# Performance work log

Hardware: AMD Instinct MI355X
Metric: run time of the kernel (lower is better)

Reference implementation:

```python
import jax, jax.numpy as jnp
import numpy as np

S, B, H, N = 512, 32, 512, 131072  # seq_len, batch, hidden_dim, num candidate spans
MAX_STEP = 20  # max_length


def setup_inputs() -> dict:
    key = jax.random.key(0)
    ks = jax.random.split(key, 8)
    hidden = jax.random.normal(ks[0], (S, B, 2 * H), dtype=jnp.float32)
    span_bids = jax.random.randint(ks[1], (N,), 0, B, dtype=jnp.int32)
    # begin in [1, S-1-MAX_STEP-1] so that begin-1>=0 and end=begin+step <= S-1
    span_begins = jax.random.randint(ks[2], (N,), 1, S - MAX_STEP - 2, dtype=jnp.int32)
    steps = jax.random.randint(ks[3], (N,), 2, MAX_STEP + 1, dtype=jnp.int32)
    span_ends = span_begins + steps
    span_flags = jax.random.randint(ks[4], (N,), 0, 2, dtype=jnp.int32)
    span_weights = jax.random.uniform(ks[5], (N,), dtype=jnp.float32)
    W1 = jax.random.normal(ks[6], (2 * H, H), dtype=jnp.float32) / np.sqrt(2.0 * H)
    b1 = jnp.zeros((H,), dtype=jnp.float32)
    W2 = jax.random.normal(ks[7], (H, 1), dtype=jnp.float32) / np.sqrt(float(H))
    b2 = jnp.zeros((1,), dtype=jnp.float32)
    return {"hidden": hidden, "span_bids": span_bids, "span_begins": span_begins,
            "span_ends": span_ends, "span_flags": span_flags, "span_weights": span_weights,
            "W1": W1, "b1": b1, "W2": W2, "b2": b2}


def reference(hidden, span_bids, span_begins, span_ends, span_flags, span_weights, W1, b1, W2, b2):
    h = W2.shape[0]  # hidden_dim
    # vectorized _span_embed: fwd diff on first half, bwd diff on second half
    fwd = hidden[span_ends - 1, span_bids, :h] - hidden[span_begins - 1, span_bids, :h]
    bwd = hidden[span_begins, span_bids, h:] - hidden[span_ends, span_bids, h:]
    feats = jnp.concatenate([fwd, bwd], axis=-1)  # [N, 2H]
    z = jnp.maximum(feats @ W1 + b1, 0.0)
    p = jax.nn.sigmoid(z @ W2 + b2)[:, 0]  # [N]
    targets = (span_flags == 1).astype(p.dtype)
    n_pos = jnp.sum(targets)
    n_tot = jnp.asarray(targets.shape[0], p.dtype)
    scale = 2.0 * n_pos / n_tot  # negative weights scaled by 2*P/(P+N)
    w_eff = jnp.where(span_flags == 1, span_weights, span_weights * scale)
    pc = jnp.clip(p, 1e-7, 1.0 - 1e-7)
    bce = -(targets * jnp.log(pc) + (1.0 - targets) * jnp.log(1.0 - pc))
    loss = jnp.mean(w_eff * bce)
    return loss
```

## Files before the change

### kernel.cpp

```cpp
#include <hip/hip_runtime.h>
#include <hip/hip_bf16.h>


typedef float f32x4 __attribute__((ext_vector_type(4)));
typedef float f32x2 __attribute__((ext_vector_type(2)));
typedef __bf16 bf16x8 __attribute__((ext_vector_type(8)));
typedef __bf16 bf16x4 __attribute__((ext_vector_type(4)));

__device__ __forceinline__ unsigned short f2bf(float f) {
  unsigned int u = __float_as_uint(f);
  u += 0x7fffu + ((u >> 16) & 1u);
  return (unsigned short)(u >> 16);
}
__device__ __forceinline__ float bf2f(unsigned int lo16) {
  return __uint_as_float(lo16 << 16);
}

__global__ void prep(const float* __restrict__ W1,
                     unsigned short* __restrict__ W1b,
                     const int* __restrict__ bids, int* __restrict__ ghist,
                     int nspans) {
  __shared__ int h[32];
  int t = threadIdx.x;
  if (blockIdx.x < 256) {
    int idx = blockIdx.x * 256 + t;
    int kc = idx & 3;
    int n  = (idx >> 2) & 511;
    int c  = idx >> 11;
    int k0 = c * 32 + kc * 8;
    unsigned short tmp[8];
#pragma unroll
    for (int j = 0; j < 8; ++j)
      tmp[j] = f2bf(W1[(k0 + j) * 512 + n]);
    *(uint4*)(W1b + c * 16384 + n * 32 + kc * 8) = *(uint4*)tmp;
  } else {
    if (t < 32) h[t] = 0;
    __syncthreads();
    int base = (blockIdx.x - 256) * 1024;
#pragma unroll
    for (int i = 0; i < 4; ++i) {
      int idx = base + t + i * 256;
      if (idx < nspans) atomicAdd(&h[bids[idx]], 1);
    }
    __syncthreads();
    if (t < 32) atomicAdd(&ghist[t], h[t]);
  }
}

__global__ void span_scatter(const int* __restrict__ bids,
                             const int* __restrict__ ghist,
                             int* __restrict__ gslot,
                             int* __restrict__ sidx, int nspans) {
  __shared__ int lh[32], lbase[32], lcur[32];
  int t = threadIdx.x;
  if (t < 32) lh[t] = 0;
  __syncthreads();
  int base = blockIdx.x * 512;
  int myb[2];
#pragma unroll
  for (int i = 0; i < 2; ++i) {
    int idx = base + t + i * 256;
    myb[i] = (idx < nspans) ? bids[idx] : -1;
    if (myb[i] >= 0) atomicAdd(&lh[myb[i]], 1);
  }
  __syncthreads();
  if (t < 32) {
    int pre = 0;
    for (int j = 0; j < t; ++j) pre += ghist[j];
    lbase[t] = pre + atomicAdd(&gslot[t], lh[t]);
    lcur[t] = 0;
  }
  __syncthreads();
#pragma unroll
  for (int i = 0; i < 2; ++i) {
    int b = myb[i];
    if (b >= 0) {
      int pos = lbase[b] + atomicAdd(&lcur[b], 1);
      sidx[pos] = base + t + i * 256;
    }
  }
}

__global__ __launch_bounds__(512, 4) void proj_gemm(
    const float* __restrict__ hidden,
    const unsigned short* __restrict__ w1b,
    unsigned char* __restrict__ Wq) {
  __shared__ __align__(16) unsigned short LB[32768];

  const int t = threadIdx.x;
  const int lane = t & 63;
  const int w = t >> 6;
  const int r0 = blockIdx.x << 6;
  const int hk = blockIdx.y << 9;
  const int q = lane >> 4;
  const int m = lane & 15;

  {
    const int kq = lane >> 4;
    const int sm = lane & 15;
#pragma unroll
    for (int ii = 0; ii < 2; ++ii) {
      const int it = (w << 1) + ii;
#pragma unroll
      for (int mt = 0; mt < 4; ++mt) {
#pragma unroll
        for (int hh = 0; hh < 2; ++hh) {
          const int kk_ = (hh << 4) + (kq << 2);
          const float* gp = hidden + ((r0 + (mt << 4) + sm) << 10)
                                   + hk + (it << 5) + kk_;
          float4 f = *(const float4*)gp;
          bf16x4 hv;
          hv[0] = (__bf16)f.x; hv[1] = (__bf16)f.y;
          hv[2] = (__bf16)f.z; hv[3] = (__bf16)f.w;
          const int qq = kk_ >> 3;
          const int kkr = kk_ & 7;
          *(bf16x4*)(LB + (((it << 2) + mt) << 9)
                        + (((qq << 4) + sm) << 3) + kkr) = hv;
        }
      }
    }
  }
  __syncthreads();

  int boffn[4];
#pragma unroll
  for (int nt = 0; nt < 4; ++nt)
    boffn[nt] = (((w << 6) + (nt << 4) + m) << 5) + (q << 3);
  const unsigned short* w1base = w1b + (blockIdx.y << 18);

  f32x4 acc[4][4];
#pragma unroll
  for (int i = 0; i < 4; ++i)
#pragma unroll
    for (int j = 0; j < 4; ++j) acc[i][j] = (f32x4){0.f, 0.f, 0.f, 0.f};

#pragma unroll
  for (int it = 0; it < 16; ++it) {
    const unsigned short* bt = w1base + (it << 14);
    bf16x8 bfr[4];
#pragma unroll
    for (int nt = 0; nt < 4; ++nt)
      bfr[nt] = *(const bf16x8*)(bt + boffn[nt]);
    bf16x8 af[4];
#pragma unroll
    for (int mt = 0; mt < 4; ++mt)
      af[mt] = *(const bf16x8*)(LB + (((it << 2) + mt) << 9)
                                   + (((q << 4) + m) << 3));
#pragma unroll
    for (int mt = 0; mt < 4; ++mt)
#pragma unroll
      for (int nt = 0; nt < 4; ++nt)
        acc[mt][nt] = __builtin_amdgcn_mfma_f32_16x16x32_bf16(af[mt], bfr[nt],
                                                              acc[mt][nt], 0, 0, 0);
  }

  {
    const int cb = (w << 6) + (m << 2);
#pragma unroll
    for (int mt = 0; mt < 4; ++mt) {
#pragma unroll
      for (int r = 0; r < 4; ++r) {
        unsigned int o = __builtin_amdgcn_cvt_pk_fp8_f32(
            acc[mt][0][r], acc[mt][1][r], 0, false);
        o = __builtin_amdgcn_cvt_pk_fp8_f32(
            acc[mt][2][r], acc[mt][3][r], o, true);
        int grow = r0 + (mt << 4) + (q << 2) + r;
        if (hk == 0) {
          *(unsigned int*)(Wq + (grow << 10) + cb) = o;
        } else if (grow >= 32) {
          *(unsigned int*)(Wq + ((grow - 32) << 10) + 512 + cb) = o;
        }
      }
    }
  }
}

#define SPB 64
#define CHUNKS 4
__global__ __launch_bounds__(256) void span_eval(
    const unsigned char* __restrict__ Wq,
    const int* __restrict__ sidx,
    const int* __restrict__ bids, const int* __restrict__ begins,
    const int* __restrict__ ends, const int* __restrict__ flags,
    const float* __restrict__ weights,
    const float* __restrict__ b1, const float* __restrict__ w2,
    const float* __restrict__ b2, float* __restrict__ partials) {
  __shared__ int oB[2][SPB], oE[2][SPB], sfl[2][SPB];
  __shared__ float swt[2][SPB];
  __shared__ float red[4][3];
  const int t = threadIdx.x;
  const int lane = t & 63;
  const int w = t >> 6;
  const int h = lane >> 5;
  const int hl = lane & 31;

  const int nblk = gridDim.x;
  int lb = blockIdx.x;
  if ((nblk & 7) == 0) {
    const int cpx = nblk >> 3;
    lb = (blockIdx.x & 7) * cpx + (blockIdx.x >> 3);
  }
  const int base0 = lb * (SPB * CHUNKS);

  auto ldmeta = [&](int c) {
    if (t < SPB) {
      int s = sidx[base0 + c * SPB + t];
      int b = bids[s], bg = begins[s], en = ends[s];
      int p = c & 1;
      oB[p][t] = (((bg - 1) << 5) + b) << 10;
      oE[p][t] = (((en - 1) << 5) + b) << 10;
      sfl[p][t] = flags[s];
      swt[p][t] = weights[s];
    }
  };
  ldmeta(0);

  const int sp0 = ((w << 1) + h) << 3;
  const int c0 = hl << 4;
  f32x2 b1p[8], w2p[8];
#pragma unroll
  for (int i = 0; i < 8; ++i) {
#pragma unroll
    for (int j2 = 0; j2 < 2; ++j2) {
      int j = 2 * i + j2;
      int colp = ((hl >> 2) << 6) + ((j & 3) << 4) + ((hl & 3) << 2) + (j >> 2);
      b1p[i][j2] = b1[colp];
      w2p[i][j2] = w2[colp];
    }
  }
  const float b2v = b2[0];
  __syncthreads();

  auto dec2 = [](unsigned int v, f32x2* f) {
    f[0] = __builtin_amdgcn_cvt_pk_f32_fp8(v, false);
    f[1] = __builtin_amdgcn_cvt_pk_f32_fp8(v, true);
  };

  const f32x2 zero2 = (f32x2){0.f, 0.f};
  float pos_t = 0.f, neg_t = 0.f, cnt_t = 0.f;

  for (int c = 0; c < CHUNKS; ++c) {
    const int cur = c & 1;
    uint4 BU[4], BV[4], EU[4], EV[4];
    auto ld = [&](int slot, int j) {
      int ob = oB[cur][sp0 + j], oe = oE[cur][sp0 + j];
      BU[slot] = *(const uint4*)(Wq + ob + c0);
      BV[slot] = *(const uint4*)(Wq + ob + 512 + c0);
      EU[slot] = *(const uint4*)(Wq + oe + c0);
      EV[slot] = *(const uint4*)(Wq + oe + 512 + c0);
    };
    ld(0, 0); ld(1, 1); ld(2, 2); ld(3, 3);
    if (c + 1 < CHUNKS) ldmeta(c + 1);

    float mylogit = 0.f;
#pragma unroll
    for (int j = 0; j < 8; ++j) {
      const int slot = j & 3;
      f32x2 bu2[8], bv2[8], eu2[8], ev2[8];
      dec2(BU[slot].x, bu2 + 0); dec2(BU[slot].y, bu2 + 2);
      dec2(BU[slot].z, bu2 + 4); dec2(BU[slot].w, bu2 + 6);
      dec2(BV[slot].x, bv2 + 0); dec2(BV[slot].y, bv2 + 2);
      dec2(BV[slot].z, bv2 + 4); dec2(BV[slot].w, bv2 + 6);
      dec2(EU[slot].x, eu2 + 0); dec2(EU[slot].y, eu2 + 2);
      dec2(EU[slot].z, eu2 + 4); dec2(EU[slot].w, eu2 + 6);
      dec2(EV[slot].x, ev2 + 0); dec2(EV[slot].y, ev2 + 2);
      dec2(EV[slot].z, ev2 + 4); dec2(EV[slot].w, ev2 + 6);
      if (j + 4 < 8) ld(slot, j + 4);
      f32x2 sv2 = zero2;
#pragma unroll
      for (int i = 0; i < 8; ++i) {
        f32x2 zp = eu2[i] - bu2[i] + bv2[i] - ev2[i] + b1p[i];
        zp = __builtin_elementwise_max(zp, zero2);
        sv2 = sv2 + zp * w2p[i];
      }
      float sv = sv2[0] + sv2[1];
      sv += __shfl_xor(sv, 1);
      sv += __shfl_xor(sv, 2);
      sv += __shfl_xor(sv, 4);
      sv += __shfl_xor(sv, 8);
      sv += __shfl_xor(sv, 16);
      if (hl == j) mylogit = sv;
    }

    mylogit = __shfl(mylogit, ((lane & 8) << 2) + (lane & 7));

    if (lane < 16) {
      int sl = (w << 4) + lane;
      float logit = mylogit + b2v;
      float p = 1.f / (1.f + expf(-logit));
      p = fminf(fmaxf(p, 1e-7f), 1.f - 1e-7f);
      int fl = sfl[cur][sl];
      float bce = (fl == 1) ? -logf(p) : -logf(1.f - p);
      float term = swt[cur][sl] * bce;
      pos_t += (fl == 1) ? term : 0.f;
      neg_t += (fl == 1) ? 0.f : term;
      cnt_t += (fl == 1) ? 1.f : 0.f;
    }
    __syncthreads();
  }

#pragma unroll
  for (int off = 1; off < 64; off <<= 1) {
    pos_t += __shfl_xor(pos_t, off);
    neg_t += __shfl_xor(neg_t, off);
    cnt_t += __shfl_xor(cnt_t, off);
  }
  if (lane == 0) { red[w][0] = pos_t; red[w][1] = neg_t; red[w][2] = cnt_t; }
  __syncthreads();
  if (t == 0) {
    partials[(blockIdx.x << 2) + 0] = red[0][0] + red[1][0] + red[2][0] + red[3][0];
    partials[(blockIdx.x << 2) + 1] = red[0][1] + red[1][1] + red[2][1] + red[3][1];
    partials[(blockIdx.x << 2) + 2] = red[0][2] + red[1][2] + red[2][2] + red[3][2];
  }
}

__global__ void finalize(const float* __restrict__ parts, int nblk,
                         float* __restrict__ out, int nspans) {
  __shared__ float sp[4], sn[4], sc[4];
  float P = 0.f, Ng = 0.f, C = 0.f;
  for (int i = threadIdx.x; i < nblk; i += 256) {
    P += parts[(i << 2) + 0];
    Ng += parts[(i << 2) + 1];
    C += parts[(i << 2) + 2];
  }
#pragma unroll
  for (int off = 1; off < 64; off <<= 1) {
    P += __shfl_xor(P, off);
    Ng += __shfl_xor(Ng, off);
    C += __shfl_xor(C, off);
  }
  int w = threadIdx.x >> 6;
  if ((threadIdx.x & 63) == 0) { sp[w] = P; sn[w] = Ng; sc[w] = C; }
  __syncthreads();
  if (threadIdx.x == 0) {
    P = sp[0] + sp[1] + sp[2] + sp[3];
    Ng = sn[0] + sn[1] + sn[2] + sn[3];
    C = sc[0] + sc[1] + sc[2] + sc[3];
    float scale = 2.f * C / (float)nspans;
    out[0] = (P + scale * Ng) / (float)nspans;
  }
}

extern "C" void kernel_launch(void* const* d_in, const int* in_sizes, int n_in,
                              void* d_out, int out_size, void* d_ws, size_t ws_size,
                              hipStream_t stream) {
  const float* hidden = (const float*)d_in[0];
  const int* bids     = (const int*)d_in[1];
  const int* begins   = (const int*)d_in[2];
  const int* ends     = (const int*)d_in[3];
  const int* flags    = (const int*)d_in[4];
  const float* weights = (const float*)d_in[5];
  const float* W1 = (const float*)d_in[6];
  const float* b1 = (const float*)d_in[7];
  const float* W2 = (const float*)d_in[8];
  const float* b2 = (const float*)d_in[9];
  float* out = (float*)d_out;
  const int nspans = in_sizes[1];
  const int nblk = nspans / (SPB * CHUNKS);

  float* partials = (float*)d_ws;
  unsigned short* W1b = (unsigned short*)((char*)d_ws + (1 << 18));
  unsigned char* Wq = (unsigned char*)((char*)d_ws + (2 << 20));
  int* ghist = (int*)((char*)d_ws + (19 << 20));
  int* gslot = ghist + 32;
  int* sidx  = (int*)((char*)d_ws + (20 << 20));

  hipMemsetAsync(ghist, 0, 64 * sizeof(int), stream);
  prep<<<384, 256, 0, stream>>>(W1, W1b, bids, ghist, nspans);
  span_scatter<<<(nspans + 511) / 512, 256, 0, stream>>>(bids, ghist, gslot,
                                                         sidx, nspans);
  proj_gemm<<<dim3(256, 2), 512, 0, stream>>>(hidden, W1b, Wq);
  span_eval<<<nblk, 256, 0, stream>>>(Wq, sidx, bids, begins, ends, flags,
                                      weights, b1, W2, b2, partials);
  finalize<<<1, 256, 0, stream>>>(partials, nblk, out, nspans);
}
```

Baseline: 163.0 us.

## Enlarge proj_gemm tile to 128 rows with 2x4 wave grid and K chunks

The projection GEMM block now covers 128 rows instead of 64. Its 8 waves are arranged as 2 M-groups by 4 N-groups, each owning a 64x128 sub-tile, and the K dimension is staged through LDS in two chunks. This halves the number of blocks and doubles the reuse of each W1 fragment loaded from global memory, at the cost of more accumulator registers (occupancy hint lowered to 2) and an extra barrier per chunk. Separately, span_eval CHUNKS drops from 4 to 2, which doubles its grid size.

```diff
diff --git a/kernel.cpp b/kernel.cpp
--- a/kernel.cpp
+++ b/kernel.cpp
@@ -81,7 +81,7 @@
   }
 }
 
-__global__ __launch_bounds__(512, 4) void proj_gemm(
+__global__ __launch_bounds__(512, 2) void proj_gemm(
     const float* __restrict__ hidden,
     const unsigned short* __restrict__ w1b,
     unsigned char* __restrict__ Wq) {
@@ -90,85 +90,95 @@
   const int t = threadIdx.x;
   const int lane = t & 63;
   const int w = t >> 6;
-  const int r0 = blockIdx.x << 6;
+  const int mg = w >> 2;
+  const int ng = w & 3;
+  const int r0 = blockIdx.x << 7;
   const int hk = blockIdx.y << 9;
   const int q = lane >> 4;
   const int m = lane & 15;
 
-  {
-    const int kq = lane >> 4;
-    const int sm = lane & 15;
-#pragma unroll
-    for (int ii = 0; ii < 2; ++ii) {
-      const int it = (w << 1) + ii;
-#pragma unroll
-      for (int mt = 0; mt < 4; ++mt) {
+  const unsigned short* w1base = w1b + (blockIdx.y << 18);
+  int boffn[8];
+#pragma unroll
+  for (int nt = 0; nt < 8; ++nt)
+    boffn[nt] = (((ng << 7) + (nt << 4) + m) << 5) + (q << 3);
+
+  f32x4 acc[4][8];
+#pragma unroll
+  for (int i = 0; i < 4; ++i)
+#pragma unroll
+    for (int j = 0; j < 8; ++j) acc[i][j] = (f32x4){0.f, 0.f, 0.f, 0.f};
+
+  const int kq = lane >> 4;
+  const int sm = lane & 15;
+
+#pragma unroll
+  for (int chunk = 0; chunk < 2; ++chunk) {
+    {
+      const int kb = (chunk << 8) + (w << 5);
+#pragma unroll
+      for (int mtA = 0; mtA < 8; ++mtA) {
 #pragma unroll
         for (int hh = 0; hh < 2; ++hh) {
           const int kk_ = (hh << 4) + (kq << 2);
-          const float* gp = hidden + ((r0 + (mt << 4) + sm) << 10)
-                                   + hk + (it << 5) + kk_;
+          const float* gp = hidden + ((r0 + (mtA << 4) + sm) << 10)
+                                   + hk + kb + kk_;
           float4 f = *(const float4*)gp;
           bf16x4 hv;
           hv[0] = (__bf16)f.x; hv[1] = (__bf16)f.y;
           hv[2] = (__bf16)f.z; hv[3] = (__bf16)f.w;
           const int qq = kk_ >> 3;
           const int kkr = kk_ & 7;
-          *(bf16x4*)(LB + (((it << 2) + mt) << 9)
+          *(bf16x4*)(LB + (((w << 3) + mtA) << 9)
                         + (((qq << 4) + sm) << 3) + kkr) = hv;
         }
       }
     }
-  }
-  __syncthreads();
-
-  int boffn[4];
-#pragma unroll
-  for (int nt = 0; nt < 4; ++nt)
-    boffn[nt] = (((w << 6) + (nt << 4) + m) << 5) + (q << 3);
-  const unsigned short* w1base = w1b + (blockIdx.y << 18);
-
-  f32x4 acc[4][4];
-#pragma unroll
-  for (int i = 0; i < 4; ++i)
-#pragma unroll
-    for (int j = 0; j < 4; ++j) acc[i][j] = (f32x4){0.f, 0.f, 0.f, 0.f};
-
-#pragma unroll
-  for (int it = 0; it < 16; ++it) {
-    const unsigned short* bt = w1base + (it << 14);
-    bf16x8 bfr[4];
-#pragma unroll
-    for (int nt = 0; nt < 4; ++nt)
-      bfr[nt] = *(const bf16x8*)(bt + boffn[nt]);
-    bf16x8 af[4];
-#pragma unroll
-    for (int mt = 0; mt < 4; ++mt)
-      af[mt] = *(const bf16x8*)(LB + (((it << 2) + mt) << 9)
-                                   + (((q << 4) + m) << 3));
-#pragma unroll
-    for (int mt = 0; mt < 4; ++mt)
-#pragma unroll
-      for (int nt = 0; nt < 4; ++nt)
-        acc[mt][nt] = __builtin_amdgcn_mfma_f32_16x16x32_bf16(af[mt], bfr[nt],
-                                                              acc[mt][nt], 0, 0, 0);
+    __syncthreads();
+
+#pragma unroll
+    for (int itL = 0; itL < 8; ++itL) {
+      const unsigned short* bt = w1base + (((chunk << 3) + itL) << 14);
+      bf16x8 bfr[8];
+#pragma unroll
+      for (int nt = 0; nt < 8; ++nt)
+        bfr[nt] = *(const bf16x8*)(bt + boffn[nt]);
+      bf16x8 af[4];
+#pragma unroll
+      for (int mt = 0; mt < 4; ++mt)
+        af[mt] = *(const bf16x8*)(LB + (((itL << 3) + (mg << 2) + mt) << 9)
+                                     + (((q << 4) + m) << 3));
+#pragma unroll
+      for (int mt = 0; mt < 4; ++mt)
+#pragma unroll
+        for (int nt = 0; nt < 8; ++nt)
+          acc[mt][nt] = __builtin_amdgcn_mfma_f32_16x16x32_bf16(af[mt], bfr[nt],
+                                                                acc[mt][nt], 0, 0, 0);
+    }
+    __syncthreads();
   }
 
   {
-    const int cb = (w << 6) + (m << 2);
+    const int cb1 = (ng << 7) + (m << 2);
 #pragma unroll
     for (int mt = 0; mt < 4; ++mt) {
 #pragma unroll
       for (int r = 0; r < 4; ++r) {
-        unsigned int o = __builtin_amdgcn_cvt_pk_fp8_f32(
+        unsigned int o1 = __builtin_amdgcn_cvt_pk_fp8_f32(
             acc[mt][0][r], acc[mt][1][r], 0, false);
-        o = __builtin_amdgcn_cvt_pk_fp8_f32(
-            acc[mt][2][r], acc[mt][3][r], o, true);
-        int grow = r0 + (mt << 4) + (q << 2) + r;
+        o1 = __builtin_amdgcn_cvt_pk_fp8_f32(
+            acc[mt][2][r], acc[mt][3][r], o1, true);
+        unsigned int o2 = __builtin_amdgcn_cvt_pk_fp8_f32(
+            acc[mt][4][r], acc[mt][5][r], 0, false);
+        o2 = __builtin_amdgcn_cvt_pk_fp8_f32(
+            acc[mt][6][r], acc[mt][7][r], o2, true);
+        int grow = r0 + (mg << 6) + (mt << 4) + (q << 2) + r;
         if (hk == 0) {
-          *(unsigned int*)(Wq + (grow << 10) + cb) = o;
+          *(unsigned int*)(Wq + (grow << 10) + cb1) = o1;
+          *(unsigned int*)(Wq + (grow << 10) + cb1 + 64) = o2;
         } else if (grow >= 32) {
-          *(unsigned int*)(Wq + ((grow - 32) << 10) + 512 + cb) = o;
+          *(unsigned int*)(Wq + ((grow - 32) << 10) + 512 + cb1) = o1;
+          *(unsigned int*)(Wq + ((grow - 32) << 10) + 512 + cb1 + 64) = o2;
         }
       }
     }
@@ -176,7 +186,7 @@
 }
 
 #define SPB 64
-#define CHUNKS 4
+#define CHUNKS 2
 __global__ __launch_bounds__(256) void span_eval(
     const unsigned char* __restrict__ Wq,
     const int* __restrict__ sidx,
@@ -369,7 +379,7 @@
   prep<<<384, 256, 0, stream>>>(W1, W1b, bids, ghist, nspans);
   span_scatter<<<(nspans + 511) / 512, 256, 0, stream>>>(bids, ghist, gslot,
                                                          sidx, nspans);
-  proj_gemm<<<dim3(256, 2), 512, 0, stream>>>(hidden, W1b, Wq);
+  proj_gemm<<<dim3(128, 2), 512, 0, stream>>>(hidden, W1b, Wq);
   span_eval<<<nblk, 256, 0, stream>>>(Wq, sidx, bids, begins, ends, flags,
                                       weights, b1, W2, b2, partials);
   finalize<<<1, 256, 0, stream>>>(partials, nblk, out, nspans);
```

Measured after the change: 166.4 us. 1.02x slower.
